# Performance work log

Measured on AMD Instinct MI355X. Metric: run time of the kernel, lower is better.

## Reference

```python
import jax, jax.numpy as jnp
import numpy as np
import math

EMBED_DIM = 1024
NUM_HEADS = 16
B, T = 4, 2048
HEAD_DIM = EMBED_DIM // NUM_HEADS


def setup_inputs() -> dict:
    key = jax.random.key(0)
    ks = jax.random.split(key, 9)
    s = 1.0 / math.sqrt(EMBED_DIM)
    x = jax.random.normal(ks[0], (B, T, EMBED_DIM), dtype=jnp.float32)
    # causal mask, broadcastable over (B, H)
    mask = jnp.tril(jnp.ones((T, T), dtype=bool))[None, None, :, :]
    Wq = jax.random.normal(ks[1], (EMBED_DIM, EMBED_DIM), dtype=jnp.float32) * s
    bq = jnp.zeros((EMBED_DIM,), dtype=jnp.float32)
    Wk = jax.random.normal(ks[2], (EMBED_DIM, EMBED_DIM), dtype=jnp.float32) * s
    bk = jnp.zeros((EMBED_DIM,), dtype=jnp.float32)
    Wv = jax.random.normal(ks[3], (EMBED_DIM, EMBED_DIM), dtype=jnp.float32) * s
    bv = jnp.zeros((EMBED_DIM,), dtype=jnp.float32)
    Wo = jax.random.normal(ks[4], (EMBED_DIM, EMBED_DIM), dtype=jnp.float32) * s
    bo = jnp.zeros((EMBED_DIM,), dtype=jnp.float32)
    return {"x": x, "mask": mask, "Wq": Wq, "bq": bq, "Wk": Wk, "bk": bk,
            "Wv": Wv, "bv": bv, "Wo": Wo, "bo": bo}


def reference(x, mask, Wq, bq, Wk, bk, Wv, bv, Wo, bo):
    Bsz, Tlen, C = x.shape
    H, D = NUM_HEADS, HEAD_DIM
    q = (x @ Wq + bq).reshape(Bsz, Tlen, H, D).transpose(0, 2, 1, 3)  # [B,H,T,D]
    k = (x @ Wk + bk).reshape(Bsz, Tlen, H, D).transpose(0, 2, 1, 3)
    v = (x @ Wv + bv).reshape(Bsz, Tlen, H, D).transpose(0, 2, 1, 3)
    scores = jnp.einsum('bhtd,bhsd->bhts', q, k) / math.sqrt(D)  # [B,H,T,T]
    scores = jnp.where(mask, scores, jnp.float32(-1e9))
    attn = jax.nn.softmax(scores, axis=-1)
    out = jnp.einsum('bhts,bhsd->bhtd', attn, v)  # [B,H,T,D]
    out = out.transpose(0, 2, 1, 3).reshape(Bsz, Tlen, C)
    return out @ Wo + bo
```

## Files before the change

kernel.cpp:

```cpp
#include <hip/hip_runtime.h>

#define SEQ   2048
#define NH    16
#define HD    64
#define EMB   1024
#define NB    4
#define MTOT  (NB*SEQ)
#define NT    (SEQ/64)

typedef _Float16 f16;
typedef _Float16 f16x4 __attribute__((ext_vector_type(4)));
typedef _Float16 f16x8 __attribute__((ext_vector_type(8)));
typedef float    f32x4 __attribute__((ext_vector_type(4)));

#define MFMA_F16(a,b,c) __builtin_amdgcn_mfma_f32_16x16x32_f16(a,b,c,0,0,0)

#define QSCALE 0.18033688011112043f

__device__ __forceinline__ float fast_exp2(float x) {
#if __has_builtin(__builtin_amdgcn_exp2f)
  return __builtin_amdgcn_exp2f(x);
#else
  return exp2f(x);
#endif
}

__device__ __forceinline__ void gload16(const f16* g, f16* l) {
  __builtin_amdgcn_global_load_lds(
      (const __attribute__((address_space(1))) void*)g,
      (__attribute__((address_space(3))) void*)l, 16, 0, 0);
}

__global__ __launch_bounds__(256) void cast_x_kernel(
    const float* __restrict__ x, f16* __restrict__ xh) {
  size_t i = ((size_t)blockIdx.x * 256 + threadIdx.x) * 8;
  float4 a = *(const float4*)(x + i);
  float4 b = *(const float4*)(x + i + 4);
  f16x8 o;
  o[0]=(f16)a.x; o[1]=(f16)a.y; o[2]=(f16)a.z; o[3]=(f16)a.w;
  o[4]=(f16)b.x; o[5]=(f16)b.y; o[6]=(f16)b.z; o[7]=(f16)b.w;
  *(f16x8*)(xh + i) = o;
}

__global__ __launch_bounds__(256) void wtrans_kernel(
    const float* __restrict__ W0, const float* __restrict__ W1,
    const float* __restrict__ W2, const float* __restrict__ W3,
    f16* __restrict__ O0, f16* __restrict__ O1,
    f16* __restrict__ O2, f16* __restrict__ O3) {
  const int z = blockIdx.z;
  const float* W = (z==0)?W0:(z==1)?W1:(z==2)?W2:W3;
  f16* O        = (z==0)?O0:(z==1)?O1:(z==2)?O2:O3;
  __shared__ float Tl[64][68];
  const int t = threadIdx.x;
  const int k0 = blockIdx.x * 64, n0 = blockIdx.y * 64;
  {
    const int r = t >> 2, c0 = (t & 3) * 16;
    const float* src = W + (size_t)(k0 + r) * EMB + n0 + c0;
    #pragma unroll
    for (int j = 0; j < 4; ++j) {
      float4 v = *(const float4*)(src + 4 * j);
      Tl[c0+4*j+0][r]=v.x; Tl[c0+4*j+1][r]=v.y;
      Tl[c0+4*j+2][r]=v.z; Tl[c0+4*j+3][r]=v.w;
    }
  }
  __syncthreads();
  {
    const int n = t >> 2, c0 = (t & 3) * 16;
    f16* dst = O + (size_t)(n0 + n) * EMB + k0 + c0;
    #pragma unroll
    for (int j = 0; j < 2; ++j) {
      f16x8 o;
      #pragma unroll
      for (int u = 0; u < 8; ++u) o[u] = (f16)Tl[n][c0 + 8*j + u];
      *(f16x8*)(dst + 8 * j) = o;
    }
  }
}

template<int MODE>
__device__ __forceinline__ void gemm_core(
    const f16* __restrict__ A, const f16* __restrict__ Bt,
    const float* __restrict__ bias, void* __restrict__ out,
    int m0, int n0, float scale) {
  __shared__ f16 As[128 * 64];
  __shared__ f16 Bs[128 * 64];
  const int tid  = threadIdx.x;
  const int lane = tid & 63, w = tid >> 6;
  const int g = lane >> 4, lx = lane & 15;
  const int wr = w >> 1, wc = w & 1;
  const int sr = lane >> 3, sc = lane & 7;

  f32x4 acc[4][4];
  const f32x4 z4 = {0.f, 0.f, 0.f, 0.f};
  #pragma unroll
  for (int i = 0; i < 4; ++i)
    #pragma unroll
    for (int j = 0; j < 4; ++j) acc[i][j] = z4;

  for (int k0 = 0; k0 < EMB; k0 += 64) {
    __syncthreads();
    #pragma unroll
    for (int ci = 0; ci < 4; ++ci) {
      const int i = 4 * w + ci;
      const int r = i * 8 + sr;
      const int c = sc ^ (r & 7);
      gload16(A  + (size_t)(m0 + r) * EMB + k0 + c * 8, &As[i * 512]);
      gload16(Bt + (size_t)(n0 + r) * EMB + k0 + c * 8, &Bs[i * 512]);
    }
    __syncthreads();

    #pragma unroll
    for (int h = 0; h < 2; ++h) {
      f16x8 af[4], bf[4];
      #pragma unroll
      for (int mf = 0; mf < 4; ++mf) {
        const int row = wr * 64 + mf * 16 + lx;
        const int off = (row * 128 + h * 64 + g * 16) ^ ((row & 7) << 4);
        af[mf] = *(const f16x8*)((const char*)As + off);
      }
      #pragma unroll
      for (int nf = 0; nf < 4; ++nf) {
        const int row = wc * 64 + nf * 16 + lx;
        const int off = (row * 128 + h * 64 + g * 16) ^ ((row & 7) << 4);
        bf[nf] = *(const f16x8*)((const char*)Bs + off);
      }
      #pragma unroll
      for (int mf = 0; mf < 4; ++mf)
        #pragma unroll
        for (int nf = 0; nf < 4; ++nf)
          acc[mf][nf] = MFMA_F16(af[mf], bf[nf], acc[mf][nf]);
    }
  }

  #pragma unroll
  for (int mf = 0; mf < 4; ++mf) {
    #pragma unroll
    for (int nf = 0; nf < 4; ++nf) {
      const int n  = n0 + wc * 64 + nf * 16 + lx;
      const int mb = m0 + wr * 64 + mf * 16 + g * 4;
      const float bv = bias[n];
      if (MODE == 2) {
        float* op = (float*)out;
        #pragma unroll
        for (int r = 0; r < 4; ++r)
          op[(size_t)(mb + r) * EMB + n] = acc[mf][nf][r] + bv;
      } else {
        const int b = mb >> 11, tt = mb & (SEQ - 1);
        const int hh = n >> 6, d = n & (HD - 1);
        f16* op = (f16*)out;
        if (MODE == 0) {
          #pragma unroll
          for (int r = 0; r < 4; ++r)
            op[((size_t)(b * NH + hh) * SEQ + tt + r) * HD + d] =
                (f16)((acc[mf][nf][r] + bv) * scale);
        } else {
          f16x4 o;
          #pragma unroll
          for (int r = 0; r < 4; ++r) o[r] = (f16)(acc[mf][nf][r] + bv);
          *(f16x4*)(op + ((size_t)(b * NH + hh) * HD + d) * SEQ + tt) = o;
        }
      }
    }
  }
}

__global__ __launch_bounds__(256) void qkv_gemm_kernel(
    const f16* __restrict__ xh, const f16* __restrict__ wqt,
    const f16* __restrict__ wkt, const f16* __restrict__ wvt,
    const float* __restrict__ bq, const float* __restrict__ bk,
    const float* __restrict__ bv,
    f16* __restrict__ qh, f16* __restrict__ kh, f16* __restrict__ vth) {
  const int z = blockIdx.z;
  const int m0 = blockIdx.x * 128, n0 = blockIdx.y * 128;
  if (z == 0)      gemm_core<0>(xh, wqt, bq, qh, m0, n0, QSCALE);
  else if (z == 1) gemm_core<0>(xh, wkt, bk, kh, m0, n0, 1.0f);
  else             gemm_core<1>(xh, wvt, bv, vth, m0, n0, 1.0f);
}

__global__ __launch_bounds__(256) void proj_gemm_kernel(
    const f16* __restrict__ ath, const f16* __restrict__ wot,
    const float* __restrict__ bo, float* __restrict__ out) {
  gemm_core<2>(ath, wot, bo, out, blockIdx.x * 128, blockIdx.y * 128, 1.0f);
}

__global__ __launch_bounds__(256, 4) void attn_kernel(
    const f16* __restrict__ Qh, const f16* __restrict__ Kh,
    const f16* __restrict__ Vth, f16* __restrict__ Opart,
    float* __restrict__ mPart, float* __restrict__ lPart) {
  __shared__ f16 Ks[64 * 64];
  __shared__ f16 Vs[64 * 64];
  __shared__ f16 Ps[4][16 * 64];
  const int tid  = threadIdx.x;
  const int lane = tid & 63, w = tid >> 6;
  const int g = lane >> 4, lx = lane & 15;
  const int sr = lane >> 3, sc = lane & 7;
  const int bid = blockIdx.x;
  const int xcd   = bid & 7;
  const int idx   = bid >> 3;
  const int split = idx & 1;
  const int p     = (idx >> 1) & 15;
  const int bh    = xcd + 8 * (idx >> 5);
  const int qlo = p, qhi = NT - 1 - p;
  const int nkt = qhi + 1;
  const f16* qp = Qh  + (size_t)bh * SEQ * HD;
  const f16* kp = Kh  + (size_t)bh * SEQ * HD;
  const f16* vp = Vth + (size_t)bh * HD * SEQ;
  const int row0[2] = {qlo * 64 + w * 16, qhi * 64 + w * 16};

  f16x8 qf[2][2];
  #pragma unroll
  for (int part = 0; part < 2; ++part) {
    const int qrow = row0[part] + lx;
    #pragma unroll
    for (int h = 0; h < 2; ++h)
      qf[part][h] = *(const f16x8*)(qp + (size_t)qrow * HD + h * 32 + g * 8);
  }

  const f32x4 z4 = {0.f, 0.f, 0.f, 0.f};
  f32x4 oa[2][4];
  float m_i[2] = {-1e30f, -1e30f}, l_i[2] = {0.f, 0.f};
  #pragma unroll
  for (int part = 0; part < 2; ++part)
    #pragma unroll
    for (int df = 0; df < 4; ++df) oa[part][df] = z4;

  for (int kt = split; kt < nkt; kt += 2) {
    __syncthreads();
    #pragma unroll
    for (int ci = 0; ci < 2; ++ci) {
      const int i = 2 * w + ci;
      const int r = i * 8 + sr;
      const int c = sc ^ (r & 7);
      gload16(kp + (size_t)(kt * 64 + r) * HD + c * 8, &Ks[i * 512]);
      gload16(vp + (size_t)r * SEQ + kt * 64 + c * 8,  &Vs[i * 512]);
    }
    __syncthreads();

    const int npart = (kt <= qlo) ? 2 : 1;
    #pragma unroll
    for (int pi = 0; pi < 2; ++pi) {
      if (pi >= npart) continue;
      const int part = 1 - pi;
      const int qrow = row0[part] + lx;
      const bool diag = (kt == (part ? qhi : qlo));

      f32x4 sa[4];
      #pragma unroll
      for (int sf = 0; sf < 4; ++sf) sa[sf] = z4;
      __builtin_amdgcn_s_setprio(1);
      #pragma unroll
      for (int h = 0; h < 2; ++h)
        #pragma unroll
        for (int sf = 0; sf < 4; ++sf) {
          const int row = sf * 16 + lx;
          const int off = (row * 128 + h * 64 + g * 16) ^ ((row & 7) << 4);
          f16x8 kf = *(const f16x8*)((const char*)Ks + off);
          sa[sf] = MFMA_F16(kf, qf[part][h], sa[sf]);
        }
      __builtin_amdgcn_s_setprio(0);

      float rmax = -1e30f;
      #pragma unroll
      for (int sf = 0; sf < 4; ++sf)
        #pragma unroll
        for (int r = 0; r < 4; ++r) {
          float vsc = sa[sf][r];
          if (diag) {
            const int kv = kt * 64 + sf * 16 + g * 4 + r;
            if (kv > qrow) vsc = -1e30f;
          }
          sa[sf][r] = vsc;
          rmax = fmaxf(rmax, vsc);
        }
      rmax = fmaxf(rmax, __shfl_xor(rmax, 16));
      rmax = fmaxf(rmax, __shfl_xor(rmax, 32));
      const float mnew = fmaxf(m_i[part], rmax);
      const float corr = fast_exp2(m_i[part] - mnew);
      m_i[part] = mnew;
      float rsum = 0.f;
      #pragma unroll
      for (int sf = 0; sf < 4; ++sf)
        #pragma unroll
        for (int r = 0; r < 4; ++r) {
          const float pv = fast_exp2(sa[sf][r] - mnew);
          sa[sf][r] = pv;
          rsum += pv;
        }
      rsum += __shfl_xor(rsum, 16);
      rsum += __shfl_xor(rsum, 32);
      l_i[part] = l_i[part] * corr + rsum;

      #pragma unroll
      for (int sf = 0; sf < 4; ++sf) {
        f16x4 p4;
        #pragma unroll
        for (int r = 0; r < 4; ++r) p4[r] = (f16)sa[sf][r];
        const int off = (lx * 128 + sf * 32 + g * 8) ^ ((lx & 7) << 4);
        *(f16x4*)((char*)Ps[w] + off) = p4;
      }

      #pragma unroll
      for (int r = 0; r < 4; ++r) {
        const float cr = __shfl(corr, g * 4 + r, 64);
        #pragma unroll
        for (int df = 0; df < 4; ++df) oa[part][df][r] *= cr;
      }

      __builtin_amdgcn_s_setprio(1);
      #pragma unroll
      for (int hk = 0; hk < 2; ++hk) {
        const int offp = (lx * 128 + hk * 64 + g * 16) ^ ((lx & 7) << 4);
        f16x8 pf = *(const f16x8*)((const char*)Ps[w] + offp);
        #pragma unroll
        for (int df = 0; df < 4; ++df) {
          const int row = df * 16 + lx;
          const int offv = (row * 128 + hk * 64 + g * 16) ^ ((row & 7) << 4);
          f16x8 vf = *(const f16x8*)((const char*)Vs + offv);
          oa[part][df] = MFMA_F16(pf, vf, oa[part][df]);
        }
      }
      __builtin_amdgcn_s_setprio(0);
    }
  }

  const size_t sb = (size_t)split * 64 + bh;
  #pragma unroll
  for (int part = 0; part < 2; ++part) {
    if (lane < 16) {
      mPart[sb * SEQ + row0[part] + lane] = m_i[part];
      lPart[sb * SEQ + row0[part] + lane] = l_i[part];
    }
    #pragma unroll
    for (int r = 0; r < 4; ++r) {
      const int t = row0[part] + g * 4 + r;
      f16* dst = Opart + ((size_t)sb * SEQ + t) * HD;
      #pragma unroll
      for (int df = 0; df < 4; ++df)
        dst[df * 16 + lx] = (f16)(oa[part][df][r]);
    }
  }
}

__global__ __launch_bounds__(256) void combine_kernel(
    const f16* __restrict__ Opart, const float* __restrict__ mPart,
    const float* __restrict__ lPart, f16* __restrict__ Att) {
  const int G = blockIdx.x * 256 + threadIdx.x;
  const int chunk = G & 7;
  const int rowid = G >> 3;
  const int bh = rowid >> 11, t = rowid & (SEQ - 1);
  const int b = bh >> 4, h = bh & 15;
  const size_t i1 = (size_t)bh * SEQ + t;
  const size_t i2 = (size_t)(64 + bh) * SEQ + t;
  const float m1 = mPart[i1], m2 = mPart[i2];
  const float l1 = lPart[i1], l2 = lPart[i2];
  const float mx = fmaxf(m1, m2);
  const float w1 = fast_exp2(m1 - mx), w2 = fast_exp2(m2 - mx);
  const float inv = 1.f / (l1 * w1 + l2 * w2);
  const f16x8 o1 = *(const f16x8*)(Opart + i1 * HD + chunk * 8);
  const f16x8 o2 = *(const f16x8*)(Opart + i2 * HD + chunk * 8);
  f16x8 o;
  #pragma unroll
  for (int j = 0; j < 8; ++j)
    o[j] = (f16)(((float)o1[j] * w1 + (float)o2[j] * w2) * inv);
  *(f16x8*)(Att + ((size_t)b * SEQ + t) * EMB + h * HD + chunk * 8) = o;
}

extern "C" void kernel_launch(void* const* d_in, const int* in_sizes, int n_in,
                              void* d_out, int out_size, void* d_ws, size_t ws_size,
                              hipStream_t stream) {
  (void)in_sizes; (void)n_in; (void)out_size; (void)ws_size;
  const float* x  = (const float*)d_in[0];
  const float* Wq = (const float*)d_in[2];
  const float* bq = (const float*)d_in[3];
  const float* Wk = (const float*)d_in[4];
  const float* bk = (const float*)d_in[5];
  const float* Wv = (const float*)d_in[6];
  const float* bv = (const float*)d_in[7];
  const float* Wo = (const float*)d_in[8];
  const float* bo = (const float*)d_in[9];

  f16* xh    = (f16*)d_ws;
  f16* wqt   = xh  + (size_t)MTOT * EMB;
  f16* wkt   = wqt + (size_t)EMB * EMB;
  f16* wvt   = wkt + (size_t)EMB * EMB;
  f16* wot   = wvt + (size_t)EMB * EMB;
  f16* qh    = wot + (size_t)EMB * EMB;
  f16* kh    = qh  + (size_t)MTOT * EMB;
  f16* vth   = kh  + (size_t)MTOT * EMB;
  f16* ath   = vth + (size_t)MTOT * EMB;
  f16* Opart = ath + (size_t)MTOT * EMB;
  float* mP  = (float*)(Opart + (size_t)2 * 64 * SEQ * HD);
  float* lP  = mP + (size_t)2 * 64 * SEQ;

  cast_x_kernel<<<dim3(MTOT * EMB / (256 * 8)), 256, 0, stream>>>(x, xh);
  wtrans_kernel<<<dim3(16, 16, 4), 256, 0, stream>>>(
      Wq, Wk, Wv, Wo, wqt, wkt, wvt, wot);
  qkv_gemm_kernel<<<dim3(MTOT / 128, EMB / 128, 3), 256, 0, stream>>>(
      xh, wqt, wkt, wvt, bq, bk, bv, qh, kh, vth);
  attn_kernel<<<dim3((NT / 2) * 2 * NB * NH), 256, 0, stream>>>(
      qh, kh, vth, Opart, mP, lP);
  combine_kernel<<<dim3(NB * NH * SEQ * 8 / 256), 256, 0, stream>>>(
      Opart, mP, lP, ath);
  proj_gemm_kernel<<<dim3(MTOT / 128, EMB / 128), 256, 0, stream>>>(
      ath, wot, bo, (float*)d_out);
}
```

Before: 192.5 us.

## Fuse split-KV combine into output projection GEMM and merge prep kernels

Removes the combine kernel by precomputing per-row combine weights in a small kernel and having the output projection GEMM read both partial attention outputs, blend them, and write the f16 tile into shared memory. The separate cast and weight-transpose kernels are also merged into one launch. This saves the round trip of the combined attention tensor through global memory and one launch. In exchange, the A-tile load moves from async global-to-LDS copies to register loads that read twice the data and do arithmetic, repeated for every N-tile block, and the LDS stores may hit bank conflicts.

```diff
diff --git a/kernel.cpp b/kernel.cpp
--- a/kernel.cpp
+++ b/kernel.cpp
@@ -31,48 +31,52 @@
       (__attribute__((address_space(3))) void*)l, 16, 0, 0);
 }
 
-__global__ __launch_bounds__(256) void cast_x_kernel(
-    const float* __restrict__ x, f16* __restrict__ xh) {
-  size_t i = ((size_t)blockIdx.x * 256 + threadIdx.x) * 8;
-  float4 a = *(const float4*)(x + i);
-  float4 b = *(const float4*)(x + i + 4);
-  f16x8 o;
-  o[0]=(f16)a.x; o[1]=(f16)a.y; o[2]=(f16)a.z; o[3]=(f16)a.w;
-  o[4]=(f16)b.x; o[5]=(f16)b.y; o[6]=(f16)b.z; o[7]=(f16)b.w;
-  *(f16x8*)(xh + i) = o;
-}
-
-__global__ __launch_bounds__(256) void wtrans_kernel(
+__global__ __launch_bounds__(256) void prep_kernel(
+    const float* __restrict__ x, f16* __restrict__ xh,
     const float* __restrict__ W0, const float* __restrict__ W1,
     const float* __restrict__ W2, const float* __restrict__ W3,
     f16* __restrict__ O0, f16* __restrict__ O1,
     f16* __restrict__ O2, f16* __restrict__ O3) {
   const int z = blockIdx.z;
-  const float* W = (z==0)?W0:(z==1)?W1:(z==2)?W2:W3;
-  f16* O        = (z==0)?O0:(z==1)?O1:(z==2)?O2:O3;
-  __shared__ float Tl[64][68];
-  const int t = threadIdx.x;
-  const int k0 = blockIdx.x * 64, n0 = blockIdx.y * 64;
-  {
-    const int r = t >> 2, c0 = (t & 3) * 16;
-    const float* src = W + (size_t)(k0 + r) * EMB + n0 + c0;
-    #pragma unroll
-    for (int j = 0; j < 4; ++j) {
-      float4 v = *(const float4*)(src + 4 * j);
-      Tl[c0+4*j+0][r]=v.x; Tl[c0+4*j+1][r]=v.y;
-      Tl[c0+4*j+2][r]=v.z; Tl[c0+4*j+3][r]=v.w;
-    }
-  }
-  __syncthreads();
-  {
-    const int n = t >> 2, c0 = (t & 3) * 16;
-    f16* dst = O + (size_t)(n0 + n) * EMB + k0 + c0;
-    #pragma unroll
-    for (int j = 0; j < 2; ++j) {
+  if (z < 4) {
+    const float* W = (z==0)?W0:(z==1)?W1:(z==2)?W2:W3;
+    f16* O        = (z==0)?O0:(z==1)?O1:(z==2)?O2:O3;
+    __shared__ float Tl[64][68];
+    const int t = threadIdx.x;
+    const int k0 = blockIdx.x * 64, n0 = blockIdx.y * 64;
+    {
+      const int r = t >> 2, c0 = (t & 3) * 16;
+      const float* src = W + (size_t)(k0 + r) * EMB + n0 + c0;
+      #pragma unroll
+      for (int j = 0; j < 4; ++j) {
+        float4 v = *(const float4*)(src + 4 * j);
+        Tl[c0+4*j+0][r]=v.x; Tl[c0+4*j+1][r]=v.y;
+        Tl[c0+4*j+2][r]=v.z; Tl[c0+4*j+3][r]=v.w;
+      }
+    }
+    __syncthreads();
+    {
+      const int n = t >> 2, c0 = (t & 3) * 16;
+      f16* dst = O + (size_t)(n0 + n) * EMB + k0 + c0;
+      #pragma unroll
+      for (int j = 0; j < 2; ++j) {
+        f16x8 o;
+        #pragma unroll
+        for (int u = 0; u < 8; ++u) o[u] = (f16)Tl[n][c0 + 8*j + u];
+        *(f16x8*)(dst + 8 * j) = o;
+      }
+    }
+  } else {
+    const int blk = (z - 4) * 256 + blockIdx.y * 16 + blockIdx.x;
+    #pragma unroll
+    for (int it = 0; it < 8; ++it) {
+      size_t i = (((size_t)blk * 8 + it) * 256 + threadIdx.x) * 8;
+      float4 a = *(const float4*)(x + i);
+      float4 b = *(const float4*)(x + i + 4);
       f16x8 o;
-      #pragma unroll
-      for (int u = 0; u < 8; ++u) o[u] = (f16)Tl[n][c0 + 8*j + u];
-      *(f16x8*)(dst + 8 * j) = o;
+      o[0]=(f16)a.x; o[1]=(f16)a.y; o[2]=(f16)a.z; o[3]=(f16)a.w;
+      o[4]=(f16)b.x; o[5]=(f16)b.y; o[6]=(f16)b.z; o[7]=(f16)b.w;
+      *(f16x8*)(xh + i) = o;
     }
   }
 }
@@ -81,7 +85,8 @@
 __device__ __forceinline__ void gemm_core(
     const f16* __restrict__ A, const f16* __restrict__ Bt,
     const float* __restrict__ bias, void* __restrict__ out,
-    int m0, int n0, float scale) {
+    int m0, int n0, float scale,
+    const float* __restrict__ C1, const float* __restrict__ C2) {
   __shared__ f16 As[128 * 64];
   __shared__ f16 Bs[128 * 64];
   const int tid  = threadIdx.x;
@@ -104,7 +109,21 @@
       const int i = 4 * w + ci;
       const int r = i * 8 + sr;
       const int c = sc ^ (r & 7);
-      gload16(A  + (size_t)(m0 + r) * EMB + k0 + c * 8, &As[i * 512]);
+      if (MODE == 3) {
+        const int m = m0 + r;
+        const int b = m >> 11, t = m & (SEQ - 1);
+        const size_t row = (size_t)(b * NH + (k0 >> 6)) * SEQ + t;
+        const f16x8 o1 = *(const f16x8*)(A + row * HD + c * 8);
+        const f16x8 o2 = *(const f16x8*)(A + (size_t)64 * SEQ * HD + row * HD + c * 8);
+        const float c1 = C1[row], c2 = C2[row];
+        f16x8 a;
+        #pragma unroll
+        for (int j = 0; j < 8; ++j)
+          a[j] = (f16)(c1 * (float)o1[j] + c2 * (float)o2[j]);
+        *(f16x8*)((char*)As + i * 1024 + sr * 128 + sc * 16) = a;
+      } else {
+        gload16(A + (size_t)(m0 + r) * EMB + k0 + c * 8, &As[i * 512]);
+      }
       gload16(Bt + (size_t)(n0 + r) * EMB + k0 + c * 8, &Bs[i * 512]);
     }
     __syncthreads();
@@ -139,7 +158,7 @@
       const int n  = n0 + wc * 64 + nf * 16 + lx;
       const int mb = m0 + wr * 64 + mf * 16 + g * 4;
       const float bv = bias[n];
-      if (MODE == 2) {
+      if (MODE == 2 || MODE == 3) {
         float* op = (float*)out;
         #pragma unroll
         for (int r = 0; r < 4; ++r)
@@ -172,15 +191,30 @@
     f16* __restrict__ qh, f16* __restrict__ kh, f16* __restrict__ vth) {
   const int z = blockIdx.z;
   const int m0 = blockIdx.x * 128, n0 = blockIdx.y * 128;
-  if (z == 0)      gemm_core<0>(xh, wqt, bq, qh, m0, n0, QSCALE);
-  else if (z == 1) gemm_core<0>(xh, wkt, bk, kh, m0, n0, 1.0f);
-  else             gemm_core<1>(xh, wvt, bv, vth, m0, n0, 1.0f);
-}
-
-__global__ __launch_bounds__(256) void proj_gemm_kernel(
-    const f16* __restrict__ ath, const f16* __restrict__ wot,
-    const float* __restrict__ bo, float* __restrict__ out) {
-  gemm_core<2>(ath, wot, bo, out, blockIdx.x * 128, blockIdx.y * 128, 1.0f);
+  if (z == 0)      gemm_core<0>(xh, wqt, bq, qh, m0, n0, QSCALE, nullptr, nullptr);
+  else if (z == 1) gemm_core<0>(xh, wkt, bk, kh, m0, n0, 1.0f, nullptr, nullptr);
+  else             gemm_core<1>(xh, wvt, bv, vth, m0, n0, 1.0f, nullptr, nullptr);
+}
+
+__global__ __launch_bounds__(256) void proj_fused_kernel(
+    const f16* __restrict__ Opart, const f16* __restrict__ wot,
+    const float* __restrict__ bo, const float* __restrict__ C1,
+    const float* __restrict__ C2, float* __restrict__ out) {
+  gemm_core<3>(Opart, wot, bo, out, blockIdx.x * 128, blockIdx.y * 128, 1.0f,
+               C1, C2);
+}
+
+__global__ __launch_bounds__(256) void lweight_kernel(
+    const float* __restrict__ mP, const float* __restrict__ lP,
+    float* __restrict__ C1, float* __restrict__ C2) {
+  const int i = blockIdx.x * 256 + threadIdx.x;
+  const float m1 = mP[i], m2 = mP[i + 64 * SEQ];
+  const float l1 = lP[i], l2 = lP[i + 64 * SEQ];
+  const float mx = fmaxf(m1, m2);
+  const float w1 = fast_exp2(m1 - mx), w2 = fast_exp2(m2 - mx);
+  const float inv = 1.f / (l1 * w1 + l2 * w2);
+  C1[i] = w1 * inv;
+  C2[i] = w2 * inv;
 }
 
 __global__ __launch_bounds__(256, 4) void attn_kernel(
@@ -341,30 +375,6 @@
   }
 }
 
-__global__ __launch_bounds__(256) void combine_kernel(
-    const f16* __restrict__ Opart, const float* __restrict__ mPart,
-    const float* __restrict__ lPart, f16* __restrict__ Att) {
-  const int G = blockIdx.x * 256 + threadIdx.x;
-  const int chunk = G & 7;
-  const int rowid = G >> 3;
-  const int bh = rowid >> 11, t = rowid & (SEQ - 1);
-  const int b = bh >> 4, h = bh & 15;
-  const size_t i1 = (size_t)bh * SEQ + t;
-  const size_t i2 = (size_t)(64 + bh) * SEQ + t;
-  const float m1 = mPart[i1], m2 = mPart[i2];
-  const float l1 = lPart[i1], l2 = lPart[i2];
-  const float mx = fmaxf(m1, m2);
-  const float w1 = fast_exp2(m1 - mx), w2 = fast_exp2(m2 - mx);
-  const float inv = 1.f / (l1 * w1 + l2 * w2);
-  const f16x8 o1 = *(const f16x8*)(Opart + i1 * HD + chunk * 8);
-  const f16x8 o2 = *(const f16x8*)(Opart + i2 * HD + chunk * 8);
-  f16x8 o;
-  #pragma unroll
-  for (int j = 0; j < 8; ++j)
-    o[j] = (f16)(((float)o1[j] * w1 + (float)o2[j] * w2) * inv);
-  *(f16x8*)(Att + ((size_t)b * SEQ + t) * EMB + h * HD + chunk * 8) = o;
-}
-
 extern "C" void kernel_launch(void* const* d_in, const int* in_sizes, int n_in,
                               void* d_out, int out_size, void* d_ws, size_t ws_size,
                               hipStream_t stream) {
@@ -387,20 +397,19 @@
   f16* qh    = wot + (size_t)EMB * EMB;
   f16* kh    = qh  + (size_t)MTOT * EMB;
   f16* vth   = kh  + (size_t)MTOT * EMB;
-  f16* ath   = vth + (size_t)MTOT * EMB;
-  f16* Opart = ath + (size_t)MTOT * EMB;
+  f16* Opart = vth + (size_t)MTOT * EMB;
   float* mP  = (float*)(Opart + (size_t)2 * 64 * SEQ * HD);
   float* lP  = mP + (size_t)2 * 64 * SEQ;
-
-  cast_x_kernel<<<dim3(MTOT * EMB / (256 * 8)), 256, 0, stream>>>(x, xh);
-  wtrans_kernel<<<dim3(16, 16, 4), 256, 0, stream>>>(
-      Wq, Wk, Wv, Wo, wqt, wkt, wvt, wot);
+  float* C1  = lP + (size_t)2 * 64 * SEQ;
+  float* C2  = C1 + (size_t)64 * SEQ;
+
+  prep_kernel<<<dim3(16, 16, 6), 256, 0, stream>>>(
+      x, xh, Wq, Wk, Wv, Wo, wqt, wkt, wvt, wot);
   qkv_gemm_kernel<<<dim3(MTOT / 128, EMB / 128, 3), 256, 0, stream>>>(
       xh, wqt, wkt, wvt, bq, bk, bv, qh, kh, vth);
   attn_kernel<<<dim3((NT / 2) * 2 * NB * NH), 256, 0, stream>>>(
       qh, kh, vth, Opart, mP, lP);
-  combine_kernel<<<dim3(NB * NH * SEQ * 8 / 256), 256, 0, stream>>>(
-      Opart, mP, lP, ath);
-  proj_gemm_kernel<<<dim3(MTOT / 128, EMB / 128), 256, 0, stream>>>(
-      ath, wot, bo, (float*)d_out);
-}
+  lweight_kernel<<<dim3(64 * SEQ / 256), 256, 0, stream>>>(mP, lP, C1, C2);
+  proj_fused_kernel<<<dim3(MTOT / 128, EMB / 128), 256, 0, stream>>>(
+      Opart, wot, bo, C1, C2, (float*)d_out);
+}
```

Result: no change. 194.6 us (+1.1%).
